# Performance work log

Hardware: AMD Instinct MI355X
Metric: run time of the kernel (lower is better)

The kernel has to match this reference:

```python
import jax, jax.numpy as jnp
import numpy as np

B, H, Q, K, D = 2, 8, 512, 512, 64


def setup_inputs() -> dict:
    key = jax.random.key(0)
    ks = jax.random.split(key, 8)
    s = 1.0 / np.sqrt(D)
    return {
        "query": jax.random.normal(ks[0], (B, H, Q, D), dtype=jnp.float32),
        "keys": jax.random.normal(ks[1], (B, H, K, D), dtype=jnp.float32),
        "Wa_w": jax.random.normal(ks[2], (D, D), dtype=jnp.float32) * s,
        "Wa_b": jax.random.normal(ks[3], (D,), dtype=jnp.float32) * s,
        "Ua_w": jax.random.normal(ks[4], (D, D), dtype=jnp.float32) * s,
        "Ua_b": jax.random.normal(ks[5], (D,), dtype=jnp.float32) * s,
        "V_w": jax.random.normal(ks[6], (D,), dtype=jnp.float32) * s,
        "V_b": jax.random.normal(ks[7], (1,), dtype=jnp.float32) * s,
    }


def reference(query, keys, Wa_w, Wa_b, Ua_w, Ua_b, V_w, V_b):
    # Linear projections (torch Linear: x @ W.T + b)
    q_proj = jnp.einsum("bhqd,ed->bhqe", query, Wa_w) + Wa_b  # [B,H,Q,D]
    k_proj = jnp.einsum("bhkd,ed->bhke", keys, Ua_w) + Ua_b   # [B,H,K,D]
    # Broadcast add + tanh -> [B,H,Q,K,D] (the fusion-headroom intermediate)
    features = jnp.tanh(q_proj[:, :, :, None, :] + k_proj[:, :, None, :, :])
    # Linear reduce D -> scalar, squeeze last dim
    scores = jnp.einsum("bhqkd,d->bhqk", features, V_w) + V_b[0]  # [B,H,Q,K]
    return scores
```

## Files before the change

### kernel.cpp

```cpp
#include <hip/hip_runtime.h>


#define BHX 16
#define SEQ 512
#define DDIM 64
#define QT 32
#define KT 64

typedef float f4 __attribute__((ext_vector_type(4)));

__global__ __launch_bounds__(256) void proj_kernel(
    const float* __restrict__ query, const float* __restrict__ keys,
    const float* __restrict__ Wa_w,  const float* __restrict__ Wa_b,
    const float* __restrict__ Ua_w,  const float* __restrict__ Ua_b,
    float* __restrict__ eq, float* __restrict__ gk)
{
  const int t = threadIdx.x, lane = t & 63, wave = t >> 6;
  const bool is_k = blockIdx.x >= 512;
  const float* __restrict__ X  = is_k ? keys : query;
  const float* __restrict__ W  = is_k ? Ua_w : Wa_w;
  const float* __restrict__ Bv = is_k ? Ua_b : Wa_b;
  float* __restrict__ out      = is_k ? gk : eq;
  const int row0 = (blockIdx.x & 511) * 16;

  float w[64];
  const float4* W4 = (const float4*)(W + lane * DDIM);
#pragma unroll
  for (int i = 0; i < 16; ++i) {
    float4 v = W4[i];
    w[4*i] = v.x; w[4*i+1] = v.y; w[4*i+2] = v.z; w[4*i+3] = v.w;
  }
#pragma unroll
  for (int i = 0; i < 16; ++i)
    asm volatile("" : "+v"(w[4*i]), "+v"(w[4*i+1]), "+v"(w[4*i+2]), "+v"(w[4*i+3]));

  const float C = 2.885390081777926815f;
  const float b = Bv[lane];

#pragma unroll 1
  for (int i = 0; i < 4; ++i) {
    const int r   = row0 + wave * 4 + i;
    const int off = __builtin_amdgcn_readfirstlane(r * DDIM);
    const float* xr = X + off;
    float a0 = 0, a1 = 0, a2 = 0, a3 = 0;
#pragma unroll
    for (int e = 0; e < 64; e += 4) {
      a0 = __builtin_fmaf(xr[e],     w[e],     a0);
      a1 = __builtin_fmaf(xr[e + 1], w[e + 1], a1);
      a2 = __builtin_fmaf(xr[e + 2], w[e + 2], a2);
      a3 = __builtin_fmaf(xr[e + 3], w[e + 3], a3);
    }
    float p = ((a0 + a1) + (a2 + a3)) + b;
    out[(size_t)r * DDIM + lane] = __builtin_amdgcn_exp2f(C * p);
  }
}

__global__ __launch_bounds__(256)
__attribute__((amdgpu_waves_per_eu(3)))
void score_kernel(
    const float* __restrict__ eq,
    const float* __restrict__ gk,
    const float* __restrict__ Vw,
    const float* __restrict__ Vb,
    float* __restrict__ out)
{
  __shared__ float ql[QT * DDIM];

  const int bh   = blockIdx.z;
  const int q0   = blockIdx.y * QT;
  const int k0   = blockIdx.x * KT;
  const int t    = threadIdx.x;
  const int lane = t & 63;
  const int wave = t >> 6;

  f4 G[16];
  {
    const float* ga = gk + (size_t)(bh * SEQ + k0 + lane) * DDIM;
    asm volatile("global_load_dwordx4 %0, %1, off offset:0"   : "=v"(G[0])  : "v"(ga));
    asm volatile("global_load_dwordx4 %0, %1, off offset:16"  : "=v"(G[1])  : "v"(ga));
    asm volatile("global_load_dwordx4 %0, %1, off offset:32"  : "=v"(G[2])  : "v"(ga));
    asm volatile("global_load_dwordx4 %0, %1, off offset:48"  : "=v"(G[3])  : "v"(ga));
    asm volatile("global_load_dwordx4 %0, %1, off offset:64"  : "=v"(G[4])  : "v"(ga));
    asm volatile("global_load_dwordx4 %0, %1, off offset:80"  : "=v"(G[5])  : "v"(ga));
    asm volatile("global_load_dwordx4 %0, %1, off offset:96"  : "=v"(G[6])  : "v"(ga));
    asm volatile("global_load_dwordx4 %0, %1, off offset:112" : "=v"(G[7])  : "v"(ga));
    asm volatile("global_load_dwordx4 %0, %1, off offset:128" : "=v"(G[8])  : "v"(ga));
    asm volatile("global_load_dwordx4 %0, %1, off offset:144" : "=v"(G[9])  : "v"(ga));
    asm volatile("global_load_dwordx4 %0, %1, off offset:160" : "=v"(G[10]) : "v"(ga));
    asm volatile("global_load_dwordx4 %0, %1, off offset:176" : "=v"(G[11]) : "v"(ga));
    asm volatile("global_load_dwordx4 %0, %1, off offset:192" : "=v"(G[12]) : "v"(ga));
    asm volatile("global_load_dwordx4 %0, %1, off offset:208" : "=v"(G[13]) : "v"(ga));
    asm volatile("global_load_dwordx4 %0, %1, off offset:224" : "=v"(G[14]) : "v"(ga));
    asm volatile("global_load_dwordx4 %0, %1, off offset:240" : "=v"(G[15]) : "v"(ga));
  }

  {
    const float4* src = (const float4*)(eq + (size_t)(bh * SEQ + q0) * DDIM);
    float4* dst = (float4*)ql;
    dst[t * 2]     = src[t * 2];
    dst[t * 2 + 1] = src[t * 2 + 1];
  }

  float acc0 = Vb[0];
#pragma unroll
  for (int d = 0; d < 64; ++d) acc0 += Vw[d];

  __syncthreads();

  asm volatile("s_waitcnt vmcnt(0)"
               : "+v"(G[0]), "+v"(G[1]), "+v"(G[2]),  "+v"(G[3]),
                 "+v"(G[4]), "+v"(G[5]), "+v"(G[6]),  "+v"(G[7]),
                 "+v"(G[8]), "+v"(G[9]), "+v"(G[10]), "+v"(G[11]),
                 "+v"(G[12]),"+v"(G[13]),"+v"(G[14]), "+v"(G[15])
               :: "memory");

  const size_t obase = (size_t)(bh * SEQ + q0 + wave * 8) * SEQ + k0 + lane;

#pragma unroll 1
  for (int qi = 0; qi < 8; ++qi) {
    const float4* ev = (const float4*)(ql + (wave * 8 + qi) * DDIM);
    float accA = 0.f, accB = 0.f;
#pragma unroll
    for (int g = 0; g < 8; ++g) {
      const float4 e0 = ev[2 * g];
      const float4 e1 = ev[2 * g + 1];
      const float A0 = __builtin_fmaf(e0.x, G[2*g].x,     1.0f);
      const float A1 = __builtin_fmaf(e0.y, G[2*g].y,     1.0f);
      const float A2 = __builtin_fmaf(e0.z, G[2*g].z,     1.0f);
      const float A3 = __builtin_fmaf(e0.w, G[2*g].w,     1.0f);
      const float A4 = __builtin_fmaf(e1.x, G[2*g + 1].x, 1.0f);
      const float A5 = __builtin_fmaf(e1.y, G[2*g + 1].y, 1.0f);
      const float A6 = __builtin_fmaf(e1.z, G[2*g + 1].z, 1.0f);
      const float A7 = __builtin_fmaf(e1.w, G[2*g + 1].w, 1.0f);
      const int d = 8 * g;
      const float n01 = __builtin_fmaf(Vw[d + 1], A0, Vw[d]     * A1);
      const float n23 = __builtin_fmaf(Vw[d + 3], A2, Vw[d + 2] * A3);
      const float n45 = __builtin_fmaf(Vw[d + 5], A4, Vw[d + 4] * A5);
      const float n67 = __builtin_fmaf(Vw[d + 7], A6, Vw[d + 6] * A7);
      const float P01 = A0 * A1, P23 = A2 * A3, P45 = A4 * A5, P67 = A6 * A7;
      const float n0123 = __builtin_fmaf(n23, P01, n01 * P23);
      const float n4567 = __builtin_fmaf(n67, P45, n45 * P67);
      const float P0123 = P01 * P23, P4567 = P45 * P67;
      const float num   = __builtin_fmaf(n4567, P0123, n0123 * P4567);
      const float P     = P0123 * P4567;
      const float r     = __builtin_amdgcn_rcpf(P);
      if (g & 1) accB = __builtin_fmaf(num, r, accB);
      else       accA = __builtin_fmaf(num, r, accA);
    }
    out[obase + (size_t)qi * SEQ] = __builtin_fmaf(-2.f, accA + accB, acc0);
  }
}

extern "C" void kernel_launch(void* const* d_in, const int* in_sizes, int n_in,
                              void* d_out, int out_size, void* d_ws, size_t ws_size,
                              hipStream_t stream) {
  const float* query = (const float*)d_in[0];
  const float* keys  = (const float*)d_in[1];
  const float* Wa_w  = (const float*)d_in[2];
  const float* Wa_b  = (const float*)d_in[3];
  const float* Ua_w  = (const float*)d_in[4];
  const float* Ua_b  = (const float*)d_in[5];
  const float* V_w   = (const float*)d_in[6];
  const float* V_b   = (const float*)d_in[7];
  float* out = (float*)d_out;

  const int R = BHX * SEQ;
  float* eq = (float*)d_ws;
  float* gk = eq + (size_t)R * DDIM;

  proj_kernel<<<1024, 256, 0, stream>>>(query, keys, Wa_w, Wa_b,
                                        Ua_w, Ua_b, eq, gk);

  dim3 grid(SEQ / KT, SEQ / QT, BHX);
  score_kernel<<<grid, 256, 0, stream>>>(eq, gk, V_w, V_b, out);
}
```

Measured before the change: 48.45 us.

## Double Q tile and merge rational tanh trees to 16-wide per reciprocal

Raises the score kernel's Q tile from 32 to 64 rows, so each wave handles 16 query rows. This halves the grid and amortises the per-block key-tile load over more rows. The rational product trees are merged so one reciprocal covers 16 dimensions instead of 8, which halves the rcp count. The shared-memory reads change to float2 and launch bounds change to (256,4). The wider product of 16 terms risks overflow or precision loss in fp32, and the larger tile doubles shared memory per block.

Measured after the change: 58.59 us. 20.9% more time.

```diff
diff --git a/kernel.cpp b/kernel.cpp
--- a/kernel.cpp
+++ b/kernel.cpp
@@ -4,10 +4,11 @@
 #define BHX 16
 #define SEQ 512
 #define DDIM 64
-#define QT 32
+#define QT 64
 #define KT 64
 
 typedef float f4 __attribute__((ext_vector_type(4)));
+typedef float f2 __attribute__((ext_vector_type(2)));
 
 __global__ __launch_bounds__(256) void proj_kernel(
     const float* __restrict__ query, const float* __restrict__ keys,
@@ -55,9 +56,24 @@
   }
 }
 
-__global__ __launch_bounds__(256)
-__attribute__((amdgpu_waves_per_eu(3)))
-void score_kernel(
+__device__ __forceinline__ void tree8(const float* __restrict__ A,
+                                      const float* __restrict__ vw,
+                                      float& num, float& P)
+{
+  const float n01 = __builtin_fmaf(vw[1], A[0], vw[0] * A[1]);
+  const float n23 = __builtin_fmaf(vw[3], A[2], vw[2] * A[3]);
+  const float n45 = __builtin_fmaf(vw[5], A[4], vw[4] * A[5]);
+  const float n67 = __builtin_fmaf(vw[7], A[6], vw[6] * A[7]);
+  const float P01 = A[0] * A[1], P23 = A[2] * A[3];
+  const float P45 = A[4] * A[5], P67 = A[6] * A[7];
+  const float n0123 = __builtin_fmaf(n23, P01, n01 * P23);
+  const float n4567 = __builtin_fmaf(n67, P45, n45 * P67);
+  const float P0123 = P01 * P23, P4567 = P45 * P67;
+  num = __builtin_fmaf(n4567, P0123, n0123 * P4567);
+  P   = P0123 * P4567;
+}
+
+__global__ __launch_bounds__(256, 4) void score_kernel(
     const float* __restrict__ eq,
     const float* __restrict__ gk,
     const float* __restrict__ Vw,
@@ -97,8 +113,8 @@
   {
     const float4* src = (const float4*)(eq + (size_t)(bh * SEQ + q0) * DDIM);
     float4* dst = (float4*)ql;
-    dst[t * 2]     = src[t * 2];
-    dst[t * 2 + 1] = src[t * 2 + 1];
+#pragma unroll
+    for (int j = 0; j < 4; ++j) dst[t + 256 * j] = src[t + 256 * j];
   }
 
   float acc0 = Vb[0];
@@ -114,36 +130,26 @@
                  "+v"(G[12]),"+v"(G[13]),"+v"(G[14]), "+v"(G[15])
                :: "memory");
 
-  const size_t obase = (size_t)(bh * SEQ + q0 + wave * 8) * SEQ + k0 + lane;
+  const size_t obase = (size_t)(bh * SEQ + q0 + wave * 16) * SEQ + k0 + lane;
 
 #pragma unroll 1
-  for (int qi = 0; qi < 8; ++qi) {
-    const float4* ev = (const float4*)(ql + (wave * 8 + qi) * DDIM);
+  for (int qi = 0; qi < 16; ++qi) {
+    const f2* ev = (const f2*)(ql + (wave * 16 + qi) * DDIM);
     float accA = 0.f, accB = 0.f;
 #pragma unroll
-    for (int g = 0; g < 8; ++g) {
-      const float4 e0 = ev[2 * g];
-      const float4 e1 = ev[2 * g + 1];
-      const float A0 = __builtin_fmaf(e0.x, G[2*g].x,     1.0f);
-      const float A1 = __builtin_fmaf(e0.y, G[2*g].y,     1.0f);
-      const float A2 = __builtin_fmaf(e0.z, G[2*g].z,     1.0f);
-      const float A3 = __builtin_fmaf(e0.w, G[2*g].w,     1.0f);
-      const float A4 = __builtin_fmaf(e1.x, G[2*g + 1].x, 1.0f);
-      const float A5 = __builtin_fmaf(e1.y, G[2*g + 1].y, 1.0f);
-      const float A6 = __builtin_fmaf(e1.z, G[2*g + 1].z, 1.0f);
-      const float A7 = __builtin_fmaf(e1.w, G[2*g + 1].w, 1.0f);
-      const int d = 8 * g;
-      const float n01 = __builtin_fmaf(Vw[d + 1], A0, Vw[d]     * A1);
-      const float n23 = __builtin_fmaf(Vw[d + 3], A2, Vw[d + 2] * A3);
-      const float n45 = __builtin_fmaf(Vw[d + 5], A4, Vw[d + 4] * A5);
-      const float n67 = __builtin_fmaf(Vw[d + 7], A6, Vw[d + 6] * A7);
-      const float P01 = A0 * A1, P23 = A2 * A3, P45 = A4 * A5, P67 = A6 * A7;
-      const float n0123 = __builtin_fmaf(n23, P01, n01 * P23);
-      const float n4567 = __builtin_fmaf(n67, P45, n45 * P67);
-      const float P0123 = P01 * P23, P4567 = P45 * P67;
-      const float num   = __builtin_fmaf(n4567, P0123, n0123 * P4567);
-      const float P     = P0123 * P4567;
-      const float r     = __builtin_amdgcn_rcpf(P);
+    for (int g = 0; g < 4; ++g) {
+      float A[16];
+#pragma unroll
+      for (int j = 0; j < 8; ++j) {
+        const f2 e = ev[8 * g + j];
+        A[2*j]     = __builtin_fmaf(e.x, G[4*g + (j >> 1)][(2*j) & 3],     1.0f);
+        A[2*j + 1] = __builtin_fmaf(e.y, G[4*g + (j >> 1)][(2*j + 1) & 3], 1.0f);
+      }
+      float numA, PA, numB, PB;
+      tree8(A,     Vw + 16 * g,     numA, PA);
+      tree8(A + 8, Vw + 16 * g + 8, numB, PB);
+      const float num = __builtin_fmaf(numA, PB, numB * PA);
+      const float r   = __builtin_amdgcn_rcpf(PA * PB);
       if (g & 1) accB = __builtin_fmaf(num, r, accB);
       else       accA = __builtin_fmaf(num, r, accA);
     }
```
